# Kernel optimization log

Hardware: AMD Instinct MI355X
Metric: run time of the kernel (lower is better)

The kernel has to match this reference:

```python
import jax, jax.numpy as jnp
import numpy as np
import math

B, L, D, H = 2, 2048, 1024, 16
DT = D // H  # d_tensor per head


def setup_inputs() -> dict:
    key = jax.random.key(0)
    ks = jax.random.split(key, 14)
    s = 1.0 / math.sqrt(D)
    return {
        "Q": jax.random.normal(ks[0], (B, L, D), jnp.float32),
        "K": jax.random.normal(ks[1], (B, L, D), jnp.float32),
        "V": jax.random.normal(ks[2], (B, L, D), jnp.float32),
        "mask": jax.random.randint(ks[3], (B, L, L), 0, 2, jnp.int32),
        "attn_bias": jax.random.normal(ks[4], (1, H, L, L), jnp.float32),
        "Wq": jax.random.normal(ks[5], (D, D), jnp.float32) * s,
        "bq": jnp.zeros((D,), jnp.float32),
        "Wk": jax.random.normal(ks[6], (D, D), jnp.float32) * s,
        "bk": jnp.zeros((D,), jnp.float32),
        "Wv": jax.random.normal(ks[7], (D, D), jnp.float32) * s,
        "bv": jnp.zeros((D,), jnp.float32),
        "Wo": jax.random.normal(ks[8], (D, D), jnp.float32) * s,
        "bo": jnp.zeros((D,), jnp.float32),
    }


def _split(x):
    # (B, L, D) -> (B, H, L, DT)
    b, l, d = x.shape
    return x.reshape(b, l, H, DT).transpose(0, 2, 1, 3)


def reference(Q, K, V, mask, attn_bias, Wq, bq, Wk, bk, Wv, bv, Wo, bo):
    # Linear projections (torch nn.Linear: x @ W.T + b)
    q = _split(Q @ Wq.T + bq)  # (B, H, L, DT)
    k = _split(K @ Wk.T + bk)
    v = _split(V @ Wv.T + bv)
    scale = 1.0 / math.sqrt(DT)
    score = jnp.einsum("bhqd,bhkd->bhqk", q, k) * scale  # (B, H, L, L)
    # masked_fill(mask==0, -10000), mask broadcast over heads
    score = jnp.where(mask[:, None, :, :] == 0, jnp.float32(-10000.0), score)
    # encoder path: additive attn_bias (is_dec_layer=False)
    score = score + attn_bias
    p = jax.nn.softmax(score, axis=-1)
    out = jnp.einsum("bhqk,bhkd->bhqd", p, v)  # (B, H, L, DT)
    out = out.transpose(0, 2, 1, 3).reshape(Q.shape[0], Q.shape[1], D)
    return out @ Wo.T + bo
```

## Files before the change

kernel.cpp:

```cpp
#include <hip/hip_runtime.h>
#include <hip/hip_bf16.h>

#define NB 2
#define NL 2048
#define ND 1024
#define NH 16
#define NDT 64
#define SZE ((size_t)NB * NL * ND)
#define WSZE ((size_t)ND * ND)

typedef unsigned short u16;
typedef unsigned int u32;
typedef unsigned long long u64;

typedef __attribute__((ext_vector_type(8))) short s16x8;
typedef __attribute__((ext_vector_type(4))) float f32x4;
typedef __attribute__((ext_vector_type(4))) u16 u16x4;
typedef __attribute__((ext_vector_type(8))) u16 u16x8;

static __device__ __forceinline__ u16 f2b(float f) {
  union { float f; u32 u; } x; x.f = f;
  u32 r = x.u + 0x7fffu + ((x.u >> 16) & 1u);
  return (u16)(r >> 16);
}
static __device__ __forceinline__ u16 f2b16(float f) {
  __hip_bfloat16 h = __float2bfloat16(f);
  return *reinterpret_cast<u16*>(&h);
}

static __device__ __forceinline__ int swz(int r, int cb) {
  return r * 128 + (cb ^ ((r & 7) << 4));
}

static __device__ __forceinline__ void gl16(const void* g, void* l) {
  __builtin_amdgcn_global_load_lds(
      (const __attribute__((address_space(1))) unsigned int*)g,
      (__attribute__((address_space(3))) unsigned int*)l, 16, 0, 0);
}

static __device__ __forceinline__ u16x8 pack8(f32x4 a, f32x4 b) {
  u16x8 r;
  r[0] = f2b(a[0]); r[1] = f2b(a[1]); r[2] = f2b(a[2]); r[3] = f2b(a[3]);
  r[4] = f2b(b[0]); r[5] = f2b(b[1]); r[6] = f2b(b[2]); r[7] = f2b(b[3]);
  return r;
}

static __device__ __forceinline__ f32x4 ldg_v4(const float* p) {
  f32x4 r;
  asm volatile("global_load_dwordx4 %0, %1, off" : "=v"(r) : "v"(p) : "memory");
  return r;
}
static __device__ __forceinline__ u64 ldg_v2(const u64* p) {
  u64 r;
  asm volatile("global_load_dwordx2 %0, %1, off" : "=v"(r) : "v"(p) : "memory");
  return r;
}

__global__ __launch_bounds__(256)
void conv_k(const float* __restrict__ q, const float* __restrict__ k,
            const float* __restrict__ v, const float* __restrict__ wq,
            const float* __restrict__ wk, const float* __restrict__ wv,
            const float* __restrict__ wo, u16* __restrict__ cin,
            u16* __restrict__ cw)
{
  const int z = blockIdx.z;
  const float* s; u16* d; size_t n;
  if (z < 3) { s = (z == 0) ? q : (z == 1) ? k : v; d = cin + (size_t)z * SZE; n = SZE; }
  else { int m = z - 3; s = (m == 0) ? wq : (m == 1) ? wk : (m == 2) ? wv : wo; d = cw + (size_t)m * WSZE; n = WSZE; }
  size_t i = ((size_t)blockIdx.x * 256 + threadIdx.x) * 8;
  if (i >= n) return;
  f32x4 a = *reinterpret_cast<const f32x4*>(s + i);
  f32x4 b = *reinterpret_cast<const f32x4*>(s + i + 4);
  *reinterpret_cast<u16x8*>(d + i) = pack8(a, b);
}

__global__ __launch_bounds__(256)
void maskpack_k(const int* __restrict__ mask, u64* __restrict__ mb) {
  const int lane = threadIdx.x & 63;
  const int gw = (blockIdx.x * 256 + threadIdx.x) >> 6;
  const int nw = (gridDim.x * 256) >> 6;
  const int NCH = NB * NL * NL / 64;
  for (int c = gw; c < NCH; c += nw) {
    int v = mask[(size_t)c * 64 + lane];
    u64 bal = __ballot(v != 0);
    if (lane == 0) mb[c] = bal;
  }
}

template<int FINAL>
__global__ __launch_bounds__(256, 2)
void gemm_k(const u16* __restrict__ Abase, const u16* __restrict__ Wbase,
            const float* __restrict__ b0, const float* __restrict__ b1,
            const float* __restrict__ b2, void* __restrict__ outp)
{
  __shared__ __align__(16) u16 lA[2][128 * 64];
  __shared__ __align__(16) u16 lB[2][128 * 64];
  const int tid = threadIdx.x, lane = tid & 63, w = tid >> 6;
  const int wr = w >> 1, wc = w & 1, lrow = lane & 15, lgrp = lane >> 4;
  const int z = FINAL ? 0 : blockIdx.z;
  const u16* A = Abase + (FINAL ? (size_t)0 : (size_t)z * SZE);
  const u16* W = Wbase + (FINAL ? 3 * WSZE : (size_t)z * WSZE);
  const float* bias = FINAL ? b0 : (z == 0 ? b0 : (z == 1) ? b1 : b2);
  const int mbase = blockIdx.y * 128, nbase = blockIdx.x * 128;

  f32x4 acc[4][4] = {};

#define GSTAGE(BUF, T) do {                                                   \
  const int k0 = (T) * 64;                                                    \
  _Pragma("unroll") for (int i = 0; i < 4; ++i) {                             \
    int r = i * 32 + w * 8 + (lane >> 3);                                     \
    int cb = ((lane & 7) << 4) ^ ((r & 7) << 4);                              \
    gl16((const char*)(A + (size_t)(mbase + r) * ND + k0) + cb,               \
         (char*)lA[BUF] + i * 4096 + w * 1024);                               \
    gl16((const char*)(W + (size_t)(nbase + r) * ND + k0) + cb,               \
         (char*)lB[BUF] + i * 4096 + w * 1024);                               \
  }                                                                           \
} while (0)

#define GCOMP(BUF) do {                                                       \
  _Pragma("unroll") for (int ks = 0; ks < 2; ++ks) {                          \
    s16x8 af[4], bf[4];                                                       \
    _Pragma("unroll") for (int t = 0; t < 4; ++t) {                           \
      af[t] = *reinterpret_cast<const s16x8*>((char*)lA[BUF] + swz(wr * 64 + t * 16 + lrow, ks * 64 + lgrp * 16)); \
      bf[t] = *reinterpret_cast<const s16x8*>((char*)lB[BUF] + swz(wc * 64 + t * 16 + lrow, ks * 64 + lgrp * 16)); \
    }                                                                         \
    _Pragma("unroll") for (int mt = 0; mt < 4; ++mt)                          \
      _Pragma("unroll") for (int nt = 0; nt < 4; ++nt)                        \
        acc[mt][nt] = __builtin_amdgcn_mfma_f32_16x16x32_bf16(af[mt], bf[nt], acc[mt][nt], 0, 0, 0); \
  }                                                                           \
} while (0)

  GSTAGE(0, 0);
  __syncthreads();
  int cur = 0;
#pragma unroll 1
  for (int t = 0; t < 15; ++t) {
    GSTAGE(cur ^ 1, t + 1);
    GCOMP(cur);
    __syncthreads();
    cur ^= 1;
  }
  GCOMP(cur);

#pragma unroll
  for (int mt = 0; mt < 4; ++mt) {
#pragma unroll
    for (int nt = 0; nt < 4; ++nt) {
      int n = nbase + wc * 64 + nt * 16 + lrow;
      float bv = bias[n];
      int m0 = mbase + wr * 64 + mt * 16 + lgrp * 4;
      f32x4 a = acc[mt][nt];
      if constexpr (FINAL) {
#pragma unroll
        for (int rg = 0; rg < 4; ++rg)
          ((float*)outp)[(size_t)(m0 + rg) * ND + n] = a[rg] + bv;
      } else {
        int h = n >> 6, d = n & 63;
        if (z == 2) {
          int b = m0 >> 11, l0 = m0 & 2047;
          u16x4 ov;
#pragma unroll
          for (int rg = 0; rg < 4; ++rg) ov[rg] = f2b(a[rg] + bv);
          *reinterpret_cast<u16x4*>((u16*)outp + 2 * SZE + ((size_t)(b * NH + h) * NDT + d) * NL + l0) = ov;
        } else {
#pragma unroll
          for (int rg = 0; rg < 4; ++rg) {
            int m = m0 + rg;
            int b = m >> 11, l = m & 2047;
            ((u16*)outp)[(size_t)z * SZE + ((size_t)(b * NH + h) * NL + l) * NDT + d] = f2b(a[rg] + bv);
          }
        }
      }
    }
  }
#undef GSTAGE
#undef GCOMP
}

__global__ __launch_bounds__(256)
void attn_k(const u16* __restrict__ q, const u16* __restrict__ k,
            const u16* __restrict__ vt, const u64* __restrict__ mb,
            const float* __restrict__ bias, u16* __restrict__ ao)
{
  __shared__ __align__(16) u16 kl2[2][64 * 64];
  __shared__ __align__(16) u16 vl2[2][64 * 64];
  __shared__ __align__(16) u16 pl[4][16 * 64];

  const int tid = threadIdx.x;
  const int lane = tid & 63, w = tid >> 6;
  const int lrow = lane & 15, lgrp = lane >> 4;
  const int bid = blockIdx.x;
  const int b = bid & 1;
  const int h = (bid >> 1) & (NH - 1);
  const int qt = bid >> 5;
  const int bh = b * NH + h;
  const int qbase = qt * 64;
  const int qrow = qbase + w * 16 + lrow;

  const float L2E = 1.4426950408889634f;
  const float SC2 = 0.125f * L2E;
  const float NEGM = -10000.0f * L2E;

  s16x8 qf[2];
#pragma unroll
  for (int ks = 0; ks < 2; ++ks)
    qf[ks] = *reinterpret_cast<const s16x8*>(q + ((size_t)bh * NL + qrow) * NDT + ks * 32 + lgrp * 8);

  f32x4 o4[4] = {};
  float mrun = -3.0e38f, lrun = 0.f;

  const u64* mrow = mb + ((size_t)b * NL + qrow) * (NL / 64);
  const float* brow = bias + ((size_t)h * NL + qrow) * NL;
  u16* pw = pl[w];

  f32x4 bA[4], bB[4];
  u64 mA, mB;

#define LOADPF(BP, MM, KK) do {                                               \
  _Pragma("unroll") for (int nt = 0; nt < 4; ++nt)                            \
    BP[nt] = ldg_v4(brow + (KK) + nt * 16 + lgrp * 4);                        \
  MM = ldg_v2(mrow + ((KK) >> 6));                                            \
} while (0)

#define STAGEKV(KK, KD, VD) do {                                              \
  const char* ksrc = (const char*)(k + ((size_t)bh * NL + (KK)) * NDT);       \
  _Pragma("unroll") for (int i = 0; i < 2; ++i) {                             \
    int o = i * 4096 + w * 1024 + lane * 16;                                  \
    int r = o >> 7; int cb = (o & 127) ^ ((r & 7) << 4);                      \
    gl16(ksrc + r * 128 + cb, (char*)(KD) + i * 4096 + w * 1024);             \
    gl16((const char*)vt + (((size_t)bh * NDT + r) * NL + (KK)) * 2 + cb,     \
         (char*)(VD) + i * 4096 + w * 1024);                                  \
  }                                                                           \
} while (0)

#define TILE(KD, VD, BP, MM) do {                                             \
  float sv[4][4];                                                             \
  __builtin_amdgcn_s_setprio(1);                                              \
  _Pragma("unroll") for (int nt = 0; nt < 4; ++nt) {                          \
    f32x4 s = {};                                                             \
    _Pragma("unroll") for (int ks = 0; ks < 2; ++ks) {                        \
      s16x8 kf = *reinterpret_cast<const s16x8*>((char*)(KD) + swz(nt * 16 + lrow, ks * 64 + lgrp * 16)); \
      s = __builtin_amdgcn_mfma_f32_16x16x32_bf16(kf, qf[ks], s, 0, 0, 0);    \
    }                                                                         \
    _Pragma("unroll") for (int rg = 0; rg < 4; ++rg) {                        \
      int sh = nt * 16 + lgrp * 4 + rg;                                       \
      float t = BP[nt][rg] * L2E;                                             \
      sv[nt][rg] = ((MM >> sh) & 1ull) ? __builtin_fmaf(s[rg], SC2, t) : t + NEGM; \
    }                                                                         \
  }                                                                           \
  __builtin_amdgcn_s_setprio(0);                                              \
  float mx = sv[0][0];                                                        \
  _Pragma("unroll") for (int nt = 0; nt < 4; ++nt)                            \
    _Pragma("unroll") for (int rg = 0; rg < 4; ++rg) mx = fmaxf(mx, sv[nt][rg]); \
  mx = fmaxf(mx, __shfl_xor(mx, 16)); mx = fmaxf(mx, __shfl_xor(mx, 32));     \
  if (!__all(mx <= mrun + 8.0f)) {                                            \
    float mnew = fmaxf(mrun, mx);                                             \
    float alpha = exp2f(mrun - mnew);                                         \
    mrun = mnew;                                                              \
    lrun *= alpha;                                                            \
    _Pragma("unroll") for (int dt = 0; dt < 4; ++dt)                          \
      _Pragma("unroll") for (int rg = 0; rg < 4; ++rg) o4[dt][rg] *= alpha;   \
  }                                                                           \
  float rs = 0.f;                                                             \
  _Pragma("unroll") for (int nt = 0; nt < 4; ++nt)                            \
    _Pragma("unroll") for (int rg = 0; rg < 4; ++rg) {                        \
      float p = exp2f(sv[nt][rg] - mrun); sv[nt][rg] = p; rs += p;            \
    }                                                                         \
  rs += __shfl_xor(rs, 16); rs += __shfl_xor(rs, 32);                         \
  lrun += rs;                                                                 \
  _Pragma("unroll") for (int nt = 0; nt < 4; ++nt) {                          \
    u16x4 pk;                                                                 \
    _Pragma("unroll") for (int rg = 0; rg < 4; ++rg) pk[rg] = f2b16(sv[nt][rg]); \
    *reinterpret_cast<u16x4*>((char*)pw + swz(lrow, nt * 32 + lgrp * 8)) = pk; \
  }                                                                           \
  s16x8 pa0 = *reinterpret_cast<const s16x8*>((char*)pw + swz(lrow, lgrp * 16)); \
  s16x8 pa1 = *reinterpret_cast<const s16x8*>((char*)pw + swz(lrow, 64 + lgrp * 16)); \
  __builtin_amdgcn_s_setprio(1);                                              \
  _Pragma("unroll") for (int dt = 0; dt < 4; ++dt) {                          \
    s16x8 vf0 = *reinterpret_cast<const s16x8*>((char*)(VD) + swz(dt * 16 + lrow, lgrp * 16)); \
    o4[dt] = __builtin_amdgcn_mfma_f32_16x16x32_bf16(vf0, pa0, o4[dt], 0, 0, 0); \
    s16x8 vf1 = *reinterpret_cast<const s16x8*>((char*)(VD) + swz(dt * 16 + lrow, 64 + lgrp * 16)); \
    o4[dt] = __builtin_amdgcn_mfma_f32_16x16x32_bf16(vf1, pa1, o4[dt], 0, 0, 0); \
  }                                                                           \
  __builtin_amdgcn_s_setprio(0);                                              \
} while (0)

  STAGEKV(0, kl2[0], vl2[0]);
  LOADPF(bA, mA, 0);
  __syncthreads();

#pragma unroll 1
  for (int tt = 0; tt < NL / 64; tt += 2) {
    STAGEKV((tt + 1) * 64, kl2[1], vl2[1]);
    LOADPF(bB, mB, (tt + 1) * 64);
    TILE(kl2[0], vl2[0], bA, mA);
    __syncthreads();
    if (tt + 2 < NL / 64) {
      STAGEKV((tt + 2) * 64, kl2[0], vl2[0]);
      LOADPF(bA, mA, (tt + 2) * 64);
    }
    TILE(kl2[1], vl2[1], bB, mB);
    __syncthreads();
  }

  float inv = 1.0f / lrun;
#pragma unroll
  for (int dt = 0; dt < 4; ++dt) {
    u16x4 ov;
#pragma unroll
    for (int rg = 0; rg < 4; ++rg) ov[rg] = f2b16(o4[dt][rg] * inv);
    *reinterpret_cast<u16x4*>(ao + ((size_t)(b * NL + qrow)) * ND + h * NDT + dt * 16 + lgrp * 4) = ov;
  }
#undef LOADPF
#undef STAGEKV
#undef TILE
}

extern "C" void kernel_launch(void* const* d_in, const int* in_sizes, int n_in,
                              void* d_out, int out_size, void* d_ws, size_t ws_size,
                              hipStream_t stream)
{
  const float* Q    = (const float*)d_in[0];
  const float* K    = (const float*)d_in[1];
  const float* V    = (const float*)d_in[2];
  const int*   mask = (const int*)d_in[3];
  const float* bias = (const float*)d_in[4];
  const float* Wq   = (const float*)d_in[5];
  const float* bq   = (const float*)d_in[6];
  const float* Wk   = (const float*)d_in[7];
  const float* bk   = (const float*)d_in[8];
  const float* Wv   = (const float*)d_in[9];
  const float* bv   = (const float*)d_in[10];
  const float* Wo   = (const float*)d_in[11];
  const float* bo   = (const float*)d_in[12];

  u16* cin  = (u16*)d_ws;
  u16* cw   = cin + 3 * SZE;
  u16* qkv  = cw + 4 * WSZE;
  u64* mbit = (u64*)(qkv + 3 * SZE);
  u16* aob  = cin;

  dim3 blk(256);

  conv_k<<<dim3(2048, 1, 7), blk, 0, stream>>>(Q, K, V, Wq, Wk, Wv, Wo, cin, cw);
  maskpack_k<<<dim3(1024), blk, 0, stream>>>(mask, mbit);

  gemm_k<0><<<dim3(ND / 128, (NB * NL) / 128, 3), blk, 0, stream>>>(cin, cw, bq, bk, bv, qkv);

  attn_k<<<dim3(NB * NH * (NL / 64)), blk, 0, stream>>>(qkv, qkv + SZE, qkv + 2 * SZE, mbit, bias, aob);

  gemm_k<1><<<dim3(ND / 128, (NB * NL) / 128), blk, 0, stream>>>(aob, cw, bo, bo, bo, d_out);
}
```

Before: 268.8 us.

## Use partial vmcnt waits and raw barriers to overlap loads with compute

Replaces __syncthreads with explicit s_waitcnt vmcnt(N) plus s_barrier and sched_barrier fences in both the projection GEMM and the attention loop. The wait then covers only the older stage while the next stage's global-to-LDS loads stay in flight, and the loop tail is peeled. It also drops the s_setprio hints and swaps the library bf16 conversion for a hand-written round-to-nearest-even. The cost is hardcoded vmcnt counts that must exactly match the number of issued loads, or reads will race with incoming data.

```diff
diff --git a/kernel.cpp b/kernel.cpp
--- a/kernel.cpp
+++ b/kernel.cpp
@@ -18,14 +18,14 @@
 typedef __attribute__((ext_vector_type(4))) u16 u16x4;
 typedef __attribute__((ext_vector_type(8))) u16 u16x8;
 
+#define VW(N) asm volatile("s_waitcnt vmcnt(" #N ")" ::: "memory")
+#define SB __builtin_amdgcn_s_barrier()
+#define SCB __builtin_amdgcn_sched_barrier(0)
+
 static __device__ __forceinline__ u16 f2b(float f) {
   union { float f; u32 u; } x; x.f = f;
   u32 r = x.u + 0x7fffu + ((x.u >> 16) & 1u);
   return (u16)(r >> 16);
-}
-static __device__ __forceinline__ u16 f2b16(float f) {
-  __hip_bfloat16 h = __float2bfloat16(f);
-  return *reinterpret_cast<u16*>(&h);
 }
 
 static __device__ __forceinline__ int swz(int r, int cb) {
@@ -131,16 +131,23 @@
 } while (0)
 
   GSTAGE(0, 0);
-  __syncthreads();
-  int cur = 0;
 #pragma unroll 1
-  for (int t = 0; t < 15; ++t) {
-    GSTAGE(cur ^ 1, t + 1);
-    GCOMP(cur);
-    __syncthreads();
-    cur ^= 1;
-  }
-  GCOMP(cur);
+  for (int t = 0; t < 14; t += 2) {
+    GSTAGE(1, t + 1);
+    SCB; VW(8); SB; SCB;
+    GCOMP(0);
+    SCB; SB; SCB;
+    GSTAGE(0, t + 2);
+    SCB; VW(8); SB; SCB;
+    GCOMP(1);
+    SCB; SB; SCB;
+  }
+  GSTAGE(1, 15);
+  SCB; VW(8); SB; SCB;
+  GCOMP(0);
+  SCB; SB; SCB;
+  SCB; VW(0); SB; SCB;
+  GCOMP(1);
 
 #pragma unroll
   for (int mt = 0; mt < 4; ++mt) {
@@ -235,7 +242,6 @@
 
 #define TILE(KD, VD, BP, MM) do {                                             \
   float sv[4][4];                                                             \
-  __builtin_amdgcn_s_setprio(1);                                              \
   _Pragma("unroll") for (int nt = 0; nt < 4; ++nt) {                          \
     f32x4 s = {};                                                             \
     _Pragma("unroll") for (int ks = 0; ks < 2; ++ks) {                        \
@@ -248,7 +254,6 @@
       sv[nt][rg] = ((MM >> sh) & 1ull) ? __builtin_fmaf(s[rg], SC2, t) : t + NEGM; \
     }                                                                         \
   }                                                                           \
-  __builtin_amdgcn_s_setprio(0);                                              \
   float mx = sv[0][0];                                                        \
   _Pragma("unroll") for (int nt = 0; nt < 4; ++nt)                            \
     _Pragma("unroll") for (int rg = 0; rg < 4; ++rg) mx = fmaxf(mx, sv[nt][rg]); \
@@ -270,45 +275,49 @@
   lrun += rs;                                                                 \
   _Pragma("unroll") for (int nt = 0; nt < 4; ++nt) {                          \
     u16x4 pk;                                                                 \
-    _Pragma("unroll") for (int rg = 0; rg < 4; ++rg) pk[rg] = f2b16(sv[nt][rg]); \
+    _Pragma("unroll") for (int rg = 0; rg < 4; ++rg) pk[rg] = f2b(sv[nt][rg]); \
     *reinterpret_cast<u16x4*>((char*)pw + swz(lrow, nt * 32 + lgrp * 8)) = pk; \
   }                                                                           \
   s16x8 pa0 = *reinterpret_cast<const s16x8*>((char*)pw + swz(lrow, lgrp * 16)); \
   s16x8 pa1 = *reinterpret_cast<const s16x8*>((char*)pw + swz(lrow, 64 + lgrp * 16)); \
-  __builtin_amdgcn_s_setprio(1);                                              \
   _Pragma("unroll") for (int dt = 0; dt < 4; ++dt) {                          \
     s16x8 vf0 = *reinterpret_cast<const s16x8*>((char*)(VD) + swz(dt * 16 + lrow, lgrp * 16)); \
     o4[dt] = __builtin_amdgcn_mfma_f32_16x16x32_bf16(vf0, pa0, o4[dt], 0, 0, 0); \
     s16x8 vf1 = *reinterpret_cast<const s16x8*>((char*)(VD) + swz(dt * 16 + lrow, 64 + lgrp * 16)); \
     o4[dt] = __builtin_amdgcn_mfma_f32_16x16x32_bf16(vf1, pa1, o4[dt], 0, 0, 0); \
   }                                                                           \
-  __builtin_amdgcn_s_setprio(0);                                              \
 } while (0)
 
   STAGEKV(0, kl2[0], vl2[0]);
   LOADPF(bA, mA, 0);
-  __syncthreads();
 
 #pragma unroll 1
-  for (int tt = 0; tt < NL / 64; tt += 2) {
+  for (int tt = 0; tt < 30; tt += 2) {
     STAGEKV((tt + 1) * 64, kl2[1], vl2[1]);
     LOADPF(bB, mB, (tt + 1) * 64);
+    SCB; VW(9); SB; SCB;
     TILE(kl2[0], vl2[0], bA, mA);
-    __syncthreads();
-    if (tt + 2 < NL / 64) {
-      STAGEKV((tt + 2) * 64, kl2[0], vl2[0]);
-      LOADPF(bA, mA, (tt + 2) * 64);
-    }
+    SCB; SB; SCB;
+    STAGEKV((tt + 2) * 64, kl2[0], vl2[0]);
+    LOADPF(bA, mA, (tt + 2) * 64);
+    SCB; VW(9); SB; SCB;
     TILE(kl2[1], vl2[1], bB, mB);
-    __syncthreads();
-  }
+    SCB; SB; SCB;
+  }
+  STAGEKV(31 * 64, kl2[1], vl2[1]);
+  LOADPF(bB, mB, 31 * 64);
+  SCB; VW(9); SB; SCB;
+  TILE(kl2[0], vl2[0], bA, mA);
+  SCB; SB; SCB;
+  SCB; VW(0); SB; SCB;
+  TILE(kl2[1], vl2[1], bB, mB);
 
   float inv = 1.0f / lrun;
 #pragma unroll
   for (int dt = 0; dt < 4; ++dt) {
     u16x4 ov;
 #pragma unroll
-    for (int rg = 0; rg < 4; ++rg) ov[rg] = f2b16(o4[dt][rg] * inv);
+    for (int rg = 0; rg < 4; ++rg) ov[rg] = f2b(o4[dt][rg] * inv);
     *reinterpret_cast<u16x4*>(ao + ((size_t)(b * NL + qrow)) * ND + h * NDT + dt * 16 + lgrp * 4) = ov;
   }
 #undef LOADPF
```

New measurement: 272.6 us. About the same (+1.4%).
